# Kernel tuning notes

Measured on AMD Instinct MI355X. Metric: run time of the kernel, lower is better.

The kernel has to match this reference:

```python
import jax, jax.numpy as jnp
import numpy as np

DIM = 512          # model dim
K = 4              # max_block_size (depthwise conv kernel size)
DS = 4             # downsample_factor
BLOCKS = (1, 2, 3, 4)  # block sizes, all offset 0
MULT = 12          # lcm(1,2,3,4) = block_pad_multiple
VOCAB = 256


def setup_inputs() -> dict:
    key = jax.random.key(0)
    ks = jax.random.split(key, 7)
    x = jax.random.randint(ks[0], (4, 4096), 0, VOCAB)
    emb = jax.random.normal(ks[1], (VOCAB, DIM), dtype=jnp.float32) * 0.02
    dw_w = jax.random.normal(ks[2], (DIM, 1, K), dtype=jnp.float32) * 0.1   # depthwise conv weight [out, in/groups, k]
    dw_b = jnp.zeros((DIM,), dtype=jnp.float32)
    pw_w = jax.random.normal(ks[3], (DIM, DIM), dtype=jnp.float32) * 0.05   # 1x1 conv weight [out, in]
    pw_b = jnp.zeros((DIM,), dtype=jnp.float32)
    score_w = jax.random.normal(ks[4], (DIM,), dtype=jnp.float32) * 0.05    # Linear(dim,1)
    score_b = jnp.zeros((), dtype=jnp.float32)
    return {"x": x, "emb": emb, "dw_w": dw_w, "dw_b": dw_b,
            "pw_w": pw_w, "pw_b": pw_b, "score_w": score_w, "score_b": score_b}


def _gbst(x, emb, dw_w, dw_b, pw_w, pw_b, score_w, score_b):
    b, n = x.shape
    m = ((n + DS - 1) // DS) * DS  # next multiple of downsample factor
    xe = emb[x]  # [b, n, d]

    # positional: Pad seq end by K-1, depthwise conv1d(k=K), then 1x1 conv
    xp = jnp.pad(xe, ((0, 0), (0, K - 1), (0, 0)))
    xc = jnp.transpose(xp, (0, 2, 1))  # [b, d, n+K-1]
    y = jax.lax.conv_general_dilated(
        xc, dw_w, window_strides=(1,), padding='VALID',
        dimension_numbers=('NCH', 'OIH', 'NCH'), feature_group_count=DIM)
    y = y + dw_b[None, :, None]                       # [b, d, n]
    y = jnp.einsum('ed,bdn->bne', pw_w, y) + pw_b     # [b, n, d]

    # pad seq to multiple of lcm of block sizes
    L = ((n + MULT - 1) // MULT) * MULT
    xpad = jnp.pad(y, ((0, 0), (0, L - n), (0, 0)))   # [b, L, d]

    # multi-scale block mean pooling, broadcast back to full length
    reprs = []
    for bs in BLOCKS:
        br = xpad.reshape(b, L // bs, bs, DIM).mean(axis=2)  # [b, L/bs, d]
        reprs.append(jnp.repeat(br, bs, axis=1))             # [b, L, d]
    block_reprs = jnp.stack(reprs, axis=2)  # [b, L, nblocks, d]

    # learned block scoring + softmax over block sizes
    scores = jnp.einsum('blkd,d->blk', block_reprs, score_w) + score_b
    scores = jax.nn.softmax(scores, axis=2)  # [b, L, nblocks]

    # consensus attention over positions (inner dim = nblocks)
    sim = jnp.einsum('bik,bjk->bij', scores, scores)  # [b, L, L]
    attn = jax.nn.softmax(sim, axis=-1)
    scores = jnp.einsum('bij,bjk->bik', attn, scores)

    out = jnp.einsum('blkd,blk->bld', block_reprs, scores)  # [b, L, d]
    out = out[:, :m]
    out = out.reshape(b, m // DS, DS, DIM).mean(axis=2)     # [b, m/DS, d]
    return out


def reference(x, emb, dw_w, dw_b, pw_w, pw_b, score_w, score_b):
    return _gbst(x, emb, dw_w, dw_b, pw_w, pw_b, score_w, score_b)
```

## Files before the change

kernel.cpp:

```cpp
#include <hip/hip_runtime.h>
#include <hip/hip_bf16.h>

#define DIMD 512
#define NSEQ 4096
#define LPAD 4104
#define NCH 12
#define CH 342
#define SPLITS 8
#define PT_BK 32

#define OFF_P      0u
#define OFF_ZACC   0u
#define OFF_AACC   16416u
#define OFF_CONST  524288u
#define OFF_Y      524800u
#define OFF_PPART  524800u
#define OFF_T      8929792u
#define OFF_S      8946208u
#define OFF_S2     9011872u

__global__ __launch_bounds__(256) void k_ptable(
    const float* __restrict__ emb, const float* __restrict__ dw_w,
    const float* __restrict__ pw_w, float* __restrict__ Ppart) {
  __shared__ float As[PT_BK][68];
  __shared__ float Bs[PT_BK][68];
  const int tid = threadIdx.x;
  const int m0 = blockIdx.x * 64;
  const int e0 = blockIdx.y * 64;
  const int z  = blockIdx.z;
  const int kk = m0 >> 8;
  const int v0 = m0 & 255;
  const int srow = tid >> 3;
  const int sd4  = (tid & 7) * 4;
  const int ty = tid >> 4, tx = tid & 15;
  float c[4][4] = {};
  for (int kt = 0; kt < 64; kt += PT_BK) {
    const int d0 = z * 64 + kt;
    const float dw0 = dw_w[(d0 + sd4 + 0) * 4 + kk];
    const float dw1 = dw_w[(d0 + sd4 + 1) * 4 + kk];
    const float dw2 = dw_w[(d0 + sd4 + 2) * 4 + kk];
    const float dw3 = dw_w[(d0 + sd4 + 3) * 4 + kk];
    #pragma unroll
    for (int rr = 0; rr < 2; ++rr) {
      const int row = srow + rr * 32;
      float4 ev = *reinterpret_cast<const float4*>(&emb[(v0 + row) * DIMD + d0 + sd4]);
      As[sd4 + 0][row] = ev.x * dw0;
      As[sd4 + 1][row] = ev.y * dw1;
      As[sd4 + 2][row] = ev.z * dw2;
      As[sd4 + 3][row] = ev.w * dw3;
      float4 bv = *reinterpret_cast<const float4*>(&pw_w[(e0 + row) * DIMD + d0 + sd4]);
      Bs[sd4 + 0][row] = bv.x;
      Bs[sd4 + 1][row] = bv.y;
      Bs[sd4 + 2][row] = bv.z;
      Bs[sd4 + 3][row] = bv.w;
    }
    __syncthreads();
    #pragma unroll
    for (int q = 0; q < PT_BK; ++q) {
      float4 a = *reinterpret_cast<const float4*>(&As[q][ty * 4]);
      float4 b = *reinterpret_cast<const float4*>(&Bs[q][tx * 4]);
      c[0][0] += a.x * b.x; c[0][1] += a.x * b.y; c[0][2] += a.x * b.z; c[0][3] += a.x * b.w;
      c[1][0] += a.y * b.x; c[1][1] += a.y * b.y; c[1][2] += a.y * b.z; c[1][3] += a.y * b.w;
      c[2][0] += a.z * b.x; c[2][1] += a.z * b.y; c[2][2] += a.z * b.z; c[2][3] += a.z * b.w;
      c[3][0] += a.w * b.x; c[3][1] += a.w * b.y; c[3][2] += a.w * b.z; c[3][3] += a.w * b.w;
    }
    __syncthreads();
  }
  #pragma unroll
  for (int i = 0; i < 4; ++i) {
    *reinterpret_cast<float4*>(
        &Ppart[(size_t)z * 524288u + (m0 + ty * 4 + i) * DIMD + e0 + tx * 4]) =
        make_float4(c[i][0], c[i][1], c[i][2], c[i][3]);
  }
}

__global__ __launch_bounds__(256) void k_pcomb(
    const float* __restrict__ Ppart, float* __restrict__ P) {
  const int idx = blockIdx.x * 256 + threadIdx.x;
  const float4* p4 = reinterpret_cast<const float4*>(Ppart);
  float4 a = p4[idx];
  #pragma unroll
  for (int zz = 1; zz < SPLITS; ++zz) {
    float4 v = p4[(size_t)zz * 131072u + idx];
    a.x += v.x; a.y += v.y; a.z += v.z; a.w += v.w;
  }
  reinterpret_cast<float4*>(P)[idx] = a;
}

__global__ __launch_bounds__(256) void k_const(
    const float* __restrict__ pw_w, const float* __restrict__ pw_b,
    const float* __restrict__ dw_b, float* __restrict__ constv) {
  const int e = blockIdx.x * 256 + threadIdx.x;
  float acc = pw_b[e];
  for (int d = 0; d < DIMD; ++d) acc += pw_w[e * DIMD + d] * dw_b[d];
  constv[e] = acc;
}

__global__ __launch_bounds__(128) void k_y(
    const int* __restrict__ x, const float* __restrict__ P,
    const float* __restrict__ constv, const float* __restrict__ score_w,
    float* __restrict__ y, float* __restrict__ t_out) {
  const int b = blockIdx.y;
  const int i0 = blockIdx.x * 8;
  const int t = threadIdx.x;
  __shared__ float red[2][8];
  float4 cv = reinterpret_cast<const float4*>(constv)[t];
  float4 sw = reinterpret_cast<const float4*>(score_w)[t];
  float td[8];
  for (int r = 0; r < 8; ++r) {
    const int i = i0 + r;
    float ax = 0.f, ay = 0.f, az = 0.f, aw = 0.f;
    if (i < NSEQ) {
      ax = cv.x; ay = cv.y; az = cv.z; aw = cv.w;
      #pragma unroll
      for (int k = 0; k < 4; ++k) {
        const int pos = i + k;
        if (pos < NSEQ) {
          const int tok = x[b * NSEQ + pos];
          const float4 pv = *reinterpret_cast<const float4*>(
              &P[((unsigned)(k << 8) + tok) * DIMD + t * 4]);
          ax += pv.x; ay += pv.y; az += pv.z; aw += pv.w;
        }
      }
    }
    *reinterpret_cast<float4*>(&y[((size_t)(b * LPAD) + i) * DIMD + t * 4]) =
        make_float4(ax, ay, az, aw);
    td[r] = ax * sw.x + ay * sw.y + az * sw.z + aw * sw.w;
  }
  const int lane = t & 63, wv = t >> 6;
  #pragma unroll
  for (int r = 0; r < 8; ++r) {
    float p = td[r];
    for (int off = 32; off > 0; off >>= 1) p += __shfl_down(p, off);
    if (lane == 0) red[wv][r] = p;
  }
  __syncthreads();
  if (t < 8) t_out[b * LPAD + i0 + t] = red[0][t] + red[1][t];
}

__global__ __launch_bounds__(256) void k_s(
    const float* __restrict__ t_in, const float* __restrict__ score_b_p,
    float* __restrict__ s, float* __restrict__ Zacc, float* __restrict__ Aacc) {
  const int b = blockIdx.y;
  const int l = blockIdx.x * 256 + threadIdx.x;
  if (l >= LPAD) return;
  Zacc[b * LPAD + l] = 0.f;
  reinterpret_cast<float4*>(Aacc)[(size_t)(b * LPAD) + l] = make_float4(0.f, 0.f, 0.f, 0.f);
  const float* tb = &t_in[b * LPAD];
  const float sb = score_b_p[0];
  float p0 = tb[l] + sb;
  int j2 = l & ~1;
  float p1 = (tb[j2] + tb[j2 + 1]) * 0.5f + sb;
  int j3 = (l / 3) * 3;
  float p2 = (tb[j3] + tb[j3 + 1] + tb[j3 + 2]) * (1.0f / 3.0f) + sb;
  int j4 = l & ~3;
  float p3 = (tb[j4] + tb[j4 + 1] + tb[j4 + 2] + tb[j4 + 3]) * 0.25f + sb;
  float mx = fmaxf(fmaxf(p0, p1), fmaxf(p2, p3));
  float e0 = __expf(p0 - mx), e1 = __expf(p1 - mx);
  float e2 = __expf(p2 - mx), e3 = __expf(p3 - mx);
  float inv = 1.0f / (e0 + e1 + e2 + e3);
  *reinterpret_cast<float4*>(&s[((size_t)(b * LPAD) + l) * 4]) =
      make_float4(e0 * inv, e1 * inv, e2 * inv, e3 * inv);
}

__global__ __launch_bounds__(64) void k_attn(
    const float* __restrict__ s, float* __restrict__ Zacc,
    float* __restrict__ Aacc) {
  const int b = blockIdx.z;
  const int c = blockIdx.y;
  const int i = blockIdx.x * 64 + threadIdx.x;
  __shared__ float4 sch[CH];
  const float4* s4 = reinterpret_cast<const float4*>(s) + (size_t)b * LPAD;
  const int j0 = c * CH;
  for (int idx = threadIdx.x; idx < CH; idx += 64) sch[idx] = s4[j0 + idx];
  __syncthreads();
  if (i >= LPAD) return;
  float4 si = s4[i];
  float z0 = 0.f, z1 = 0.f;
  float a0x = 0.f, a0y = 0.f, a0z = 0.f, a0w = 0.f;
  float a1x = 0.f, a1y = 0.f, a1z = 0.f, a1w = 0.f;
  #pragma unroll 3
  for (int jj = 0; jj < CH; jj += 2) {
    float4 u = sch[jj];
    float4 v = sch[jj + 1];
    float d0 = si.x * u.x + si.y * u.y + si.z * u.z + si.w * u.w;
    float d1 = si.x * v.x + si.y * v.y + si.z * v.z + si.w * v.w;
    float e0 = __expf(d0), e1 = __expf(d1);
    z0 += e0; a0x += e0 * u.x; a0y += e0 * u.y; a0z += e0 * u.z; a0w += e0 * u.w;
    z1 += e1; a1x += e1 * v.x; a1y += e1 * v.y; a1z += e1 * v.z; a1w += e1 * v.w;
  }
  float* za = &Zacc[b * LPAD + i];
  float* aa = &Aacc[((size_t)(b * LPAD) + i) * 4];
  atomicAdd(za, z0 + z1);
  atomicAdd(aa + 0, a0x + a1x);
  atomicAdd(aa + 1, a0y + a1y);
  atomicAdd(aa + 2, a0z + a1z);
  atomicAdd(aa + 3, a0w + a1w);
}

__global__ __launch_bounds__(256) void k_s2(
    const float* __restrict__ Zacc, const float* __restrict__ Aacc,
    float* __restrict__ s2) {
  const int b = blockIdx.y;
  const int l = blockIdx.x * 256 + threadIdx.x;
  if (l >= LPAD) return;
  const size_t idx = (size_t)(b * LPAD) + l;
  float4 a = reinterpret_cast<const float4*>(Aacc)[idx];
  float inv = 1.0f / Zacc[idx];
  reinterpret_cast<float4*>(s2)[idx] =
      make_float4(a.x * inv, a.y * inv, a.z * inv, a.w * inv);
}

__global__ __launch_bounds__(128) void k_out(
    const float* __restrict__ y, const float* __restrict__ s2,
    float* __restrict__ out) {
  const int b = blockIdx.y;
  const int g = blockIdx.x;
  const int tid = threadIdx.x;
  __shared__ float coef[8];
  const int jbase = (g == 0) ? 0 : 4 * g - 2;
  if (tid == 0) {
    float cf[8] = {0.f, 0.f, 0.f, 0.f, 0.f, 0.f, 0.f, 0.f};
    const float4* s2_4 = reinterpret_cast<const float4*>(s2) + (size_t)b * LPAD;
    for (int dl = 0; dl < 4; ++dl) {
      int l = 4 * g + dl;
      float4 sv = s2_4[l];
      float sk[4] = {sv.x, sv.y, sv.z, sv.w};
      for (int k = 0; k < 4; ++k) {
        int bs = k + 1;
        int j0 = (l / bs) * bs;
        float wv = sk[k] / (float)(bs * 4);
        for (int jj = 0; jj < bs; ++jj) cf[j0 + jj - jbase] += wv;
      }
    }
    for (int r = 0; r < 8; ++r) coef[r] = cf[r];
  }
  __syncthreads();
  const float4* y4 =
      reinterpret_cast<const float4*>(y) + ((size_t)(b * LPAD) + jbase) * 128;
  float ax = 0.f, ay = 0.f, az = 0.f, aw = 0.f;
  #pragma unroll
  for (int r = 0; r < 8; ++r) {
    float cr = coef[r];
    float4 v = y4[r * 128 + tid];
    ax += cr * v.x; ay += cr * v.y; az += cr * v.z; aw += cr * v.w;
  }
  reinterpret_cast<float4*>(out)[((size_t)(b * 1024) + g) * 128 + tid] =
      make_float4(ax, ay, az, aw);
}

extern "C" void kernel_launch(void* const* d_in, const int* in_sizes, int n_in,
                              void* d_out, int out_size, void* d_ws, size_t ws_size,
                              hipStream_t stream) {
  const int* x = (const int*)d_in[0];
  const float* emb = (const float*)d_in[1];
  const float* dw_w = (const float*)d_in[2];
  const float* dw_b = (const float*)d_in[3];
  const float* pw_w = (const float*)d_in[4];
  const float* pw_b = (const float*)d_in[5];
  const float* score_w = (const float*)d_in[6];
  const float* score_b = (const float*)d_in[7];
  float* out = (float*)d_out;
  float* ws = (float*)d_ws;
  float* P      = ws + OFF_P;
  float* Zacc   = ws + OFF_ZACC;
  float* Aacc   = ws + OFF_AACC;
  float* constv = ws + OFF_CONST;
  float* y      = ws + OFF_Y;
  float* Ppart  = ws + OFF_PPART;
  float* t      = ws + OFF_T;
  float* s      = ws + OFF_S;
  float* s2     = ws + OFF_S2;

  k_ptable<<<dim3(16, 8, SPLITS), 256, 0, stream>>>(emb, dw_w, pw_w, Ppart);
  k_pcomb<<<512, 256, 0, stream>>>(Ppart, P);
  k_const<<<2, 256, 0, stream>>>(pw_w, pw_b, dw_b, constv);
  k_y<<<dim3(513, 4), 128, 0, stream>>>(x, P, constv, score_w, y, t);
  k_s<<<dim3(17, 4), 256, 0, stream>>>(t, score_b, s, Zacc, Aacc);
  k_attn<<<dim3(65, NCH, 4), 64, 0, stream>>>(s, Zacc, Aacc);
  k_s2<<<dim3(17, 4), 256, 0, stream>>>(Zacc, Aacc, s2);
  k_out<<<dim3(1024, 4), 128, 0, stream>>>(y, s2, out);
}
```

Baseline: 167.0 us.

## Store y in bf16, drop softmax denominator, fuse const and s2 kernels

The intermediate y tensor is stored as bf16 instead of fp32, halving its write and read traffic in k_y and k_out. The attention denominator Z is no longer accumulated, because the scores sum to one and so Z equals the sum of the A components; normalisation moves into k_out, which removes k_s2 and its Zacc atomics. k_const is folded into k_pcomb with vectorised loads. k_attn uses 256-thread blocks and k_out handles two groups per block, and the workspace layout is shrunk. The bf16 storage lowers the precision of y and may loosen tolerance margins.

```diff
diff --git a/kernel.cpp b/kernel.cpp
--- a/kernel.cpp
+++ b/kernel.cpp
@@ -10,14 +10,21 @@
 #define PT_BK 32
 
 #define OFF_P      0u
-#define OFF_ZACC   0u
-#define OFF_AACC   16416u
 #define OFF_CONST  524288u
-#define OFF_Y      524800u
-#define OFF_PPART  524800u
-#define OFF_T      8929792u
-#define OFF_S      8946208u
-#define OFF_S2     9011872u
+#define OFF_T      524800u
+#define OFF_S      541216u
+#define OFF_AACC   606880u
+#define OFF_Y      672544u
+#define OFF_PPART  2773792u
+
+static __device__ __forceinline__ unsigned short f2bf(float f) {
+  unsigned u = __float_as_uint(f);
+  unsigned r = (u + 0x7FFFu + ((u >> 16) & 1u)) >> 16;
+  return (unsigned short)r;
+}
+static __device__ __forceinline__ float bf2f(unsigned short h) {
+  return __uint_as_float(((unsigned)h) << 16);
+}
 
 __global__ __launch_bounds__(256) void k_ptable(
     const float* __restrict__ emb, const float* __restrict__ dw_w,
@@ -75,7 +82,9 @@
 }
 
 __global__ __launch_bounds__(256) void k_pcomb(
-    const float* __restrict__ Ppart, float* __restrict__ P) {
+    const float* __restrict__ Ppart, float* __restrict__ P,
+    const float* __restrict__ pw_w, const float* __restrict__ pw_b,
+    const float* __restrict__ dw_b, float* __restrict__ constv) {
   const int idx = blockIdx.x * 256 + threadIdx.x;
   const float4* p4 = reinterpret_cast<const float4*>(Ppart);
   float4 a = p4[idx];
@@ -85,21 +94,23 @@
     a.x += v.x; a.y += v.y; a.z += v.z; a.w += v.w;
   }
   reinterpret_cast<float4*>(P)[idx] = a;
-}
-
-__global__ __launch_bounds__(256) void k_const(
-    const float* __restrict__ pw_w, const float* __restrict__ pw_b,
-    const float* __restrict__ dw_b, float* __restrict__ constv) {
-  const int e = blockIdx.x * 256 + threadIdx.x;
-  float acc = pw_b[e];
-  for (int d = 0; d < DIMD; ++d) acc += pw_w[e * DIMD + d] * dw_b[d];
-  constv[e] = acc;
+  if (blockIdx.x < 2) {
+    const int e = blockIdx.x * 256 + threadIdx.x;
+    float acc = pw_b[e];
+    const float4* pr = reinterpret_cast<const float4*>(&pw_w[e * DIMD]);
+    const float4* db = reinterpret_cast<const float4*>(dw_b);
+    for (int d4 = 0; d4 < DIMD / 4; ++d4) {
+      float4 w = pr[d4]; float4 bb = db[d4];
+      acc += w.x * bb.x + w.y * bb.y + w.z * bb.z + w.w * bb.w;
+    }
+    constv[e] = acc;
+  }
 }
 
 __global__ __launch_bounds__(128) void k_y(
     const int* __restrict__ x, const float* __restrict__ P,
     const float* __restrict__ constv, const float* __restrict__ score_w,
-    float* __restrict__ y, float* __restrict__ t_out) {
+    unsigned short* __restrict__ y, float* __restrict__ t_out) {
   const int b = blockIdx.y;
   const int i0 = blockIdx.x * 8;
   const int t = threadIdx.x;
@@ -123,8 +134,9 @@
         }
       }
     }
-    *reinterpret_cast<float4*>(&y[((size_t)(b * LPAD) + i) * DIMD + t * 4]) =
-        make_float4(ax, ay, az, aw);
+    ushort4 o;
+    o.x = f2bf(ax); o.y = f2bf(ay); o.z = f2bf(az); o.w = f2bf(aw);
+    *reinterpret_cast<ushort4*>(&y[((size_t)(b * LPAD) + i) * DIMD + t * 4]) = o;
     td[r] = ax * sw.x + ay * sw.y + az * sw.z + aw * sw.w;
   }
   const int lane = t & 63, wv = t >> 6;
@@ -140,11 +152,10 @@
 
 __global__ __launch_bounds__(256) void k_s(
     const float* __restrict__ t_in, const float* __restrict__ score_b_p,
-    float* __restrict__ s, float* __restrict__ Zacc, float* __restrict__ Aacc) {
+    float* __restrict__ s, float* __restrict__ Aacc) {
   const int b = blockIdx.y;
   const int l = blockIdx.x * 256 + threadIdx.x;
   if (l >= LPAD) return;
-  Zacc[b * LPAD + l] = 0.f;
   reinterpret_cast<float4*>(Aacc)[(size_t)(b * LPAD) + l] = make_float4(0.f, 0.f, 0.f, 0.f);
   const float* tb = &t_in[b * LPAD];
   const float sb = score_b_p[0];
@@ -163,20 +174,18 @@
       make_float4(e0 * inv, e1 * inv, e2 * inv, e3 * inv);
 }
 
-__global__ __launch_bounds__(64) void k_attn(
-    const float* __restrict__ s, float* __restrict__ Zacc,
-    float* __restrict__ Aacc) {
+__global__ __launch_bounds__(256) void k_attn(
+    const float* __restrict__ s, float* __restrict__ Aacc) {
   const int b = blockIdx.z;
   const int c = blockIdx.y;
-  const int i = blockIdx.x * 64 + threadIdx.x;
+  const int i = blockIdx.x * 256 + threadIdx.x;
   __shared__ float4 sch[CH];
   const float4* s4 = reinterpret_cast<const float4*>(s) + (size_t)b * LPAD;
   const int j0 = c * CH;
-  for (int idx = threadIdx.x; idx < CH; idx += 64) sch[idx] = s4[j0 + idx];
+  for (int idx = threadIdx.x; idx < CH; idx += 256) sch[idx] = s4[j0 + idx];
   __syncthreads();
   if (i >= LPAD) return;
   float4 si = s4[i];
-  float z0 = 0.f, z1 = 0.f;
   float a0x = 0.f, a0y = 0.f, a0z = 0.f, a0w = 0.f;
   float a1x = 0.f, a1y = 0.f, a1z = 0.f, a1w = 0.f;
   #pragma unroll 3
@@ -186,46 +195,33 @@
     float d0 = si.x * u.x + si.y * u.y + si.z * u.z + si.w * u.w;
     float d1 = si.x * v.x + si.y * v.y + si.z * v.z + si.w * v.w;
     float e0 = __expf(d0), e1 = __expf(d1);
-    z0 += e0; a0x += e0 * u.x; a0y += e0 * u.y; a0z += e0 * u.z; a0w += e0 * u.w;
-    z1 += e1; a1x += e1 * v.x; a1y += e1 * v.y; a1z += e1 * v.z; a1w += e1 * v.w;
-  }
-  float* za = &Zacc[b * LPAD + i];
+    a0x += e0 * u.x; a0y += e0 * u.y; a0z += e0 * u.z; a0w += e0 * u.w;
+    a1x += e1 * v.x; a1y += e1 * v.y; a1z += e1 * v.z; a1w += e1 * v.w;
+  }
   float* aa = &Aacc[((size_t)(b * LPAD) + i) * 4];
-  atomicAdd(za, z0 + z1);
   atomicAdd(aa + 0, a0x + a1x);
   atomicAdd(aa + 1, a0y + a1y);
   atomicAdd(aa + 2, a0z + a1z);
   atomicAdd(aa + 3, a0w + a1w);
 }
 
-__global__ __launch_bounds__(256) void k_s2(
-    const float* __restrict__ Zacc, const float* __restrict__ Aacc,
-    float* __restrict__ s2) {
-  const int b = blockIdx.y;
-  const int l = blockIdx.x * 256 + threadIdx.x;
-  if (l >= LPAD) return;
-  const size_t idx = (size_t)(b * LPAD) + l;
-  float4 a = reinterpret_cast<const float4*>(Aacc)[idx];
-  float inv = 1.0f / Zacc[idx];
-  reinterpret_cast<float4*>(s2)[idx] =
-      make_float4(a.x * inv, a.y * inv, a.z * inv, a.w * inv);
-}
-
-__global__ __launch_bounds__(128) void k_out(
-    const float* __restrict__ y, const float* __restrict__ s2,
+__global__ __launch_bounds__(256) void k_out(
+    const unsigned short* __restrict__ y, const float* __restrict__ Aacc,
     float* __restrict__ out) {
   const int b = blockIdx.y;
-  const int g = blockIdx.x;
-  const int tid = threadIdx.x;
-  __shared__ float coef[8];
+  const int h = threadIdx.x >> 7;
+  const int tl = threadIdx.x & 127;
+  const int g = blockIdx.x * 2 + h;
+  __shared__ float coef[2][8];
   const int jbase = (g == 0) ? 0 : 4 * g - 2;
-  if (tid == 0) {
+  if (tl == 0) {
     float cf[8] = {0.f, 0.f, 0.f, 0.f, 0.f, 0.f, 0.f, 0.f};
-    const float4* s2_4 = reinterpret_cast<const float4*>(s2) + (size_t)b * LPAD;
+    const float4* a4 = reinterpret_cast<const float4*>(Aacc) + (size_t)b * LPAD;
     for (int dl = 0; dl < 4; ++dl) {
       int l = 4 * g + dl;
-      float4 sv = s2_4[l];
-      float sk[4] = {sv.x, sv.y, sv.z, sv.w};
+      float4 av = a4[l];
+      float inv = 1.0f / (av.x + av.y + av.z + av.w);
+      float sk[4] = {av.x * inv, av.y * inv, av.z * inv, av.w * inv};
       for (int k = 0; k < 4; ++k) {
         int bs = k + 1;
         int j0 = (l / bs) * bs;
@@ -233,19 +229,19 @@
         for (int jj = 0; jj < bs; ++jj) cf[j0 + jj - jbase] += wv;
       }
     }
-    for (int r = 0; r < 8; ++r) coef[r] = cf[r];
+    for (int r = 0; r < 8; ++r) coef[h][r] = cf[r];
   }
   __syncthreads();
-  const float4* y4 =
-      reinterpret_cast<const float4*>(y) + ((size_t)(b * LPAD) + jbase) * 128;
+  const unsigned short* yb = y + ((size_t)(b * LPAD) + jbase) * DIMD + tl * 4;
   float ax = 0.f, ay = 0.f, az = 0.f, aw = 0.f;
   #pragma unroll
   for (int r = 0; r < 8; ++r) {
-    float cr = coef[r];
-    float4 v = y4[r * 128 + tid];
-    ax += cr * v.x; ay += cr * v.y; az += cr * v.z; aw += cr * v.w;
-  }
-  reinterpret_cast<float4*>(out)[((size_t)(b * 1024) + g) * 128 + tid] =
+    float cr = coef[h][r];
+    ushort4 v = *reinterpret_cast<const ushort4*>(&yb[r * DIMD]);
+    ax += cr * bf2f(v.x); ay += cr * bf2f(v.y);
+    az += cr * bf2f(v.z); aw += cr * bf2f(v.w);
+  }
+  reinterpret_cast<float4*>(out)[((size_t)(b * 1024) + g) * 128 + tl] =
       make_float4(ax, ay, az, aw);
 }
 
@@ -263,21 +259,17 @@
   float* out = (float*)d_out;
   float* ws = (float*)d_ws;
   float* P      = ws + OFF_P;
-  float* Zacc   = ws + OFF_ZACC;
-  float* Aacc   = ws + OFF_AACC;
   float* constv = ws + OFF_CONST;
-  float* y      = ws + OFF_Y;
-  float* Ppart  = ws + OFF_PPART;
   float* t      = ws + OFF_T;
   float* s      = ws + OFF_S;
-  float* s2     = ws + OFF_S2;
+  float* Aacc   = ws + OFF_AACC;
+  unsigned short* y = (unsigned short*)(ws + OFF_Y);
+  float* Ppart  = ws + OFF_PPART;
 
   k_ptable<<<dim3(16, 8, SPLITS), 256, 0, stream>>>(emb, dw_w, pw_w, Ppart);
-  k_pcomb<<<512, 256, 0, stream>>>(Ppart, P);
-  k_const<<<2, 256, 0, stream>>>(pw_w, pw_b, dw_b, constv);
+  k_pcomb<<<512, 256, 0, stream>>>(Ppart, P, pw_w, pw_b, dw_b, constv);
   k_y<<<dim3(513, 4), 128, 0, stream>>>(x, P, constv, score_w, y, t);
-  k_s<<<dim3(17, 4), 256, 0, stream>>>(t, score_b, s, Zacc, Aacc);
-  k_attn<<<dim3(65, NCH, 4), 64, 0, stream>>>(s, Zacc, Aacc);
-  k_s2<<<dim3(17, 4), 256, 0, stream>>>(Zacc, Aacc, s2);
-  k_out<<<dim3(1024, 4), 128, 0, stream>>>(y, s2, out);
-}
+  k_s<<<dim3(17, 4), 256, 0, stream>>>(t, score_b, s, Aacc);
+  k_attn<<<dim3(17, NCH, 4), 256, 0, stream>>>(s, Aacc);
+  k_out<<<dim3(512, 4), 256, 0, stream>>>(y, Aacc, out);
+}
```

Result: faster. 156.3 us (-6.4%).
